# Kernel optimization log

Hardware: AMD Instinct MI355X
Metric: run time of the kernel (lower is better)

Reference implementation:

```python
import jax, jax.numpy as jnp
import numpy as np

H = 1024        # hidden_units
NH = 16         # num_heads
HD = H // NH    # head_dim = 64
B = 32
S = 500
MAX_SEQ = 500
ROPE_BASE = 10000.0


def setup_inputs() -> dict:
    key = jax.random.key(0)
    ks = jax.random.split(key, 16)
    s = 1.0 / np.sqrt(H)
    inp = {
        "query": jax.random.normal(ks[0], (B, S, H), jnp.float32),
        "key":   jax.random.normal(ks[1], (B, S, H), jnp.float32),
        "value": jax.random.normal(ks[2], (B, S, H), jnp.float32),
        "attn_mask": jax.random.randint(ks[3], (B, S), 0, 2).astype(bool),
        "Wq": jax.random.uniform(ks[4], (H, H), jnp.float32, -s, s),
        "bq": jax.random.uniform(ks[5], (H,), jnp.float32, -s, s),
        "Wk": jax.random.uniform(ks[6], (H, H), jnp.float32, -s, s),
        "bk": jax.random.uniform(ks[7], (H,), jnp.float32, -s, s),
        "Wv": jax.random.uniform(ks[8], (H, H), jnp.float32, -s, s),
        "bv": jax.random.uniform(ks[9], (H,), jnp.float32, -s, s),
        "Wo": jax.random.uniform(ks[10], (H, H), jnp.float32, -s, s),
        "bo": jax.random.uniform(ks[11], (H,), jnp.float32, -s, s),
        # rel_pos_bias embedding table: [2*max_seq_len-1, num_heads]
        "rel_emb": jax.random.normal(ks[12], (2 * MAX_SEQ - 1, NH), jnp.float32),
    }
    return inp


def _rope_tables(seq_len, head_dim, dtype):
    inv_freq = 1.0 / (ROPE_BASE ** (jnp.arange(0, head_dim, 2, dtype=jnp.float32) / head_dim))
    t = jnp.arange(seq_len, dtype=jnp.float32)
    freqs = t[:, None] * inv_freq[None, :]           # [S, HD/2]
    emb = jnp.concatenate([freqs, freqs], axis=-1)   # [S, HD]
    return jnp.cos(emb).astype(dtype), jnp.sin(emb).astype(dtype)


def _apply_rope(x, cos, sin):
    # x: [B, NH, S, HD]; even/odd slicing variant from source
    x_rot = jnp.concatenate([-x[..., 1::2], x[..., 0::2]], axis=-1)
    return x * cos + x_rot * sin


def reference(query, key, value, attn_mask, Wq, bq, Wk, bk, Wv, bv, Wo, bo, rel_emb):
    b, s, _ = query.shape
    Q = (query @ Wq.T + bq).reshape(b, s, NH, HD).transpose(0, 2, 1, 3)  # [B,NH,S,HD]
    K = (key   @ Wk.T + bk).reshape(b, s, NH, HD).transpose(0, 2, 1, 3)
    V = (value @ Wv.T + bv).reshape(b, s, NH, HD).transpose(0, 2, 1, 3)

    cos, sin = _rope_tables(s, HD, Q.dtype)  # [S,HD]
    Q = _apply_rope(Q, cos, sin)
    K = _apply_rope(K, cos, sin)

    # relative-position bias: [1, NH, S, S]
    pos = jnp.arange(s)[:, None] - jnp.arange(s)[None, :]
    rel_idx = jnp.clip(pos + MAX_SEQ - 1, 0, 2 * MAX_SEQ - 2)
    rel_bias = rel_emb[rel_idx].transpose(2, 0, 1)[None]  # [1,NH,S,S]

    # key-padding mask -> additive float mask [B,1,1,S]
    mask_bias = jnp.where(attn_mask[:, None, None, :], 0.0, -jnp.inf).astype(Q.dtype)

    scale = 1.0 / np.sqrt(HD)
    scores = jnp.einsum('bhqd,bhkd->bhqk', Q, K) * scale + mask_bias + rel_bias
    attn = jax.nn.softmax(scores, axis=-1)
    out = jnp.einsum('bhqk,bhkd->bhqd', attn, V)
    out = out.transpose(0, 2, 1, 3).reshape(b, s, H)
    out = jnp.clip(out, -30.0, 30.0)
    return out @ Wo.T + bo
```

## Files before the change

### kernel.cpp

```cpp
#include <hip/hip_runtime.h>
#include <math.h>


typedef unsigned short u16;
typedef unsigned int   u32;
typedef unsigned char  u8;
using bf16x8 = __attribute__((ext_vector_type(8))) short;
using f32x4  = __attribute__((ext_vector_type(4))) float;
using f32x2  = __attribute__((ext_vector_type(2))) float;
using u16x4  = __attribute__((ext_vector_type(4))) unsigned short;

#define DEV __device__ __forceinline__

#if __has_builtin(__builtin_amdgcn_exp2f)
#define EXP2(x) __builtin_amdgcn_exp2f(x)
#else
#define EXP2(x) exp2f(x)
#endif

DEV u16 f2bf(float f) {
  union { float f; u32 u; } c; c.f = f;
  u32 u = c.u;
  return (u16)((u + 0x7FFFu + ((u >> 16) & 1u)) >> 16);
}
DEV float bf2f(u16 h) {
  union { u32 u; float f; } c; c.u = ((u32)h) << 16;
  return c.f;
}
DEV u32 cvtpk(float a, float b) {
  u32 r;
  asm("v_cvt_pk_bf16_f32 %0, %1, %2" : "=v"(r) : "v"(a), "v"(b));
  return r;
}

DEV void async16(void* l, const void* g) {
  __builtin_amdgcn_global_load_lds(
      (__attribute__((address_space(1))) unsigned int*)g,
      (__attribute__((address_space(3))) unsigned int*)l, 16, 0, 0);
}

__global__ __launch_bounds__(512) void build_gather(const void* __restrict__ mraw,
                                                    u16* __restrict__ karr,
                                                    int* __restrict__ kept) {
  const int b = blockIdx.x;
  const int t = threadIdx.x;
  const int lane = t & 63, wave = t >> 6;
  __shared__ int s_li, s_lf;
  __shared__ int wbase[8];
  __shared__ int wpop[8];
  if (t == 0) { s_li = 0; s_lf = 0; }
  __syncthreads();
  const u32* w = (const u32*)mraw;
  int li = 0, lf = 0;
  for (int g = t; g < 4000; g += 512) {
    u32 v = w[g];
    li |= !(v == 0u || v == 1u);
    lf |= !(v == 0u || v == 0x3F800000u);
  }
  if (li) atomicOr(&s_li, 1);
  if (lf) atomicOr(&s_lf, 1);
  __syncthreads();
  const int mode = (!s_li) ? 0 : ((!s_lf) ? 1 : 2);
  int v = 0;
  if (t < 500) {
    if (mode == 0)      v = ((const int*)mraw)[b * 500 + t] != 0;
    else if (mode == 1) v = (((const float*)mraw)[b * 500 + t] != 0.0f);
    else                v = ((const u8*)mraw)[b * 500 + t] != 0;
  }
  unsigned long long bal = __ballot(v != 0);
  karr[b * 512 + t] = 0xFFFF;
  if (lane == 0) wpop[wave] = __popcll(bal);
  __syncthreads();
  if (t == 0) {
    int s = 0;
    for (int ww = 0; ww < 8; ++ww) { wbase[ww] = s; s += wpop[ww]; }
    kept[b] = s;
  }
  __syncthreads();
  if (v) {
    int rank = wbase[wave] + __popcll(bal & ((1ull << lane) - 1ull));
    karr[b * 512 + rank] = (u16)t;
  }
}

__global__ __launch_bounds__(256) void rope_table(float* __restrict__ tab) {
  int idx = blockIdx.x * 256 + threadIdx.x;
  if (idx >= 16000) return;
  int s = idx >> 5, j = idx & 31;
  float ang = (float)s * exp2f(-(float)j * 0.41524100f);
  float sn, cs;
  sincosf(ang, &sn, &cs);
  tab[idx * 2] = cs;
  tab[idx * 2 + 1] = sn;
}

__global__ __launch_bounds__(256) void cvt_w4(const float* __restrict__ w0,
                                              const float* __restrict__ w1,
                                              const float* __restrict__ w2,
                                              const float* __restrict__ w3,
                                              u16* __restrict__ dst) {
  const float* src = (blockIdx.y == 0) ? w0 : (blockIdx.y == 1) ? w1
                    : (blockIdx.y == 2) ? w2 : w3;
  int i = blockIdx.x * 256 + threadIdx.x;
  f32x4 f = *(const f32x4*)(src + (size_t)i * 4);
  u16x4 o;
  o[0] = f2bf(f[0]); o[1] = f2bf(f[1]); o[2] = f2bf(f[2]); o[3] = f2bf(f[3]);
  *(u16x4*)(dst + (size_t)blockIdx.y * 1048576 + (size_t)i * 4) = o;
}

__global__ __launch_bounds__(256) void cvt_f32_bf16(const float* __restrict__ src,
                                                    u16* __restrict__ dst, int n4) {
  int i = blockIdx.x * 256 + threadIdx.x;
  int stride = gridDim.x * 256;
  for (; i < n4; i += stride) {
    f32x4 f = *(const f32x4*)(src + (size_t)i * 4);
    u16x4 o;
    o[0] = f2bf(f[0]); o[1] = f2bf(f[1]); o[2] = f2bf(f[2]); o[3] = f2bf(f[3]);
    *(u16x4*)(dst + (size_t)i * 4) = o;
  }
}

__global__ __launch_bounds__(256) void gathercvt2(const float* __restrict__ srcK,
                                                  const float* __restrict__ srcV,
                                                  const u16* __restrict__ karr,
                                                  const int* __restrict__ kept,
                                                  u16* __restrict__ dstK,
                                                  u16* __restrict__ dstV) {
  const int b = blockIdx.y;
  const int r = blockIdx.x * 2 + (threadIdx.x >> 7);
  if (r >= kept[b]) return;
  const float* src = blockIdx.z ? srcV : srcK;
  u16* dst = blockIdx.z ? dstV : dstK;
  const int c = (threadIdx.x & 127) * 8;
  const int tok = karr[b * 512 + r];
  const float* s = src + ((size_t)b * 500 + tok) * 1024 + c;
  f32x4 f0 = *(const f32x4*)s;
  f32x4 f1 = *(const f32x4*)(s + 4);
  u16 o[8];
  o[0] = f2bf(f0[0]); o[1] = f2bf(f0[1]); o[2] = f2bf(f0[2]); o[3] = f2bf(f0[3]);
  o[4] = f2bf(f1[0]); o[5] = f2bf(f1[1]); o[6] = f2bf(f1[2]); o[7] = f2bf(f1[3]);
  *(bf16x8*)(dst + ((size_t)b * 512 + r) * 1024 + c) = *(bf16x8*)o;
}

DEV void gemm_core(const u16* __restrict__ A, size_t abase,
                   const u16* __restrict__ W,
                   int m0, int n0, int Mloc,
                   u16* AS, u16* BS, f32x4 (&acc)[4][4], int tid) {
  const int wave = tid >> 6;
  const int wr = wave >> 1, wc = wave & 1;
  const int fr = tid & 15, fo = (tid >> 4) & 3;
  const int fr2 = fr >> 1;
  const int aslot = ((4 * (fr & 1) + fo) ^ fr2) * 8;
  const int ATILE = 128 * 64;
  const int BTILE = 64 * 64;

#pragma unroll
  for (int mi = 0; mi < 4; ++mi)
#pragma unroll
    for (int ni = 0; ni < 4; ++ni)
#pragma unroll
      for (int j = 0; j < 4; ++j) acc[mi][ni][j] = 0.f;

  auto STG = [&](int t, int buf) {
    u16* sA = &AS[buf * ATILE];
    u16* sB = &BS[buf * BTILE];
#pragma unroll
    for (int i = 0; i < 2; ++i) {
      int c = i * 512 + tid;
      int r = c >> 3, v = (c & 7) ^ (r & 7);
      int ar = min(m0 + 2 * r + (v >> 2), Mloc - 1);
      async16(&sA[c * 8], A + abase + (size_t)ar * 1024 + t * 32 + (v & 3) * 8);
    }
    {
      int c = tid;
      int r = c >> 3, v = (c & 7) ^ (r & 7);
      int nr = n0 + 2 * r + (v >> 2);
      async16(&sB[c * 8], W + (size_t)nr * 1024 + t * 32 + (v & 3) * 8);
    }
  };

  STG(0, 0);
  asm volatile("s_waitcnt vmcnt(0)" ::: "memory");
  __builtin_amdgcn_sched_barrier(0);
  __builtin_amdgcn_s_barrier();

  int cur = 0;
  for (int t = 0; t < 32; ++t) {
    if (t + 1 < 32) STG(t + 1, cur ^ 1);
    const u16* a0 = &AS[cur * ATILE];
    const u16* b0 = &BS[cur * BTILE];
    bf16x8 a[4], b[4];
#pragma unroll
    for (int mi = 0; mi < 4; ++mi)
      a[mi] = *(const bf16x8*)&a0[(wr * 32 + mi * 8 + fr2) * 64 + aslot];
#pragma unroll
    for (int ni = 0; ni < 4; ++ni)
      b[ni] = *(const bf16x8*)&b0[(wc * 32 + ni * 8 + fr2) * 64 + aslot];
    asm volatile("s_waitcnt lgkmcnt(0)" ::: "memory");
    __builtin_amdgcn_sched_barrier(0);
    __builtin_amdgcn_s_setprio(1);
#pragma unroll
    for (int mi = 0; mi < 4; ++mi)
#pragma unroll
      for (int ni = 0; ni < 4; ++ni)
        acc[mi][ni] = __builtin_amdgcn_mfma_f32_16x16x32_bf16(a[mi], b[ni], acc[mi][ni], 0, 0, 0);
    __builtin_amdgcn_s_setprio(0);
    asm volatile("s_waitcnt vmcnt(0)" ::: "memory");
    __builtin_amdgcn_sched_barrier(0);
    __builtin_amdgcn_s_barrier();
    cur ^= 1;
  }
  __syncthreads();
}

__global__ __launch_bounds__(512, 4) void gemm_fused(
    const u16* __restrict__ Xq, const u16* __restrict__ XkC, const u16* __restrict__ XvC,
    const u16* __restrict__ Wb,
    const float* __restrict__ bq, const float* __restrict__ bk, const float* __restrict__ bv,
    u16* __restrict__ Qro, u16* __restrict__ Ktg, u16* __restrict__ Vtg,
    const float* __restrict__ tabg, const u16* __restrict__ karr,
    const int* __restrict__ keptp) {
  __shared__ __attribute__((aligned(16))) u16 SH[2 * 128 * 64 + 2 * 64 * 64];
  u16* AS = &SH[0];
  u16* BS = &SH[2 * 128 * 64];
  const int bid = blockIdx.x;
  const int tid = threadIdx.x;
  const int wave = tid >> 6;
  const int wr = wave >> 1, wc = wave & 1;
  const int fr = tid & 15, fo = (tid >> 4) & 3;
  const int lane = tid & 63;

  f32x4 acc[4][4];

  if (bid < 504) {
    const int swz = (bid & 7) * 63 + (bid >> 3);
    const int m0 = (swz >> 3) * 256;
    const int n0 = (swz & 7) * 128;
    gemm_core(Xq, 0, Wb, m0, n0, 16000, AS, BS, acc, tid);

    float* fw = (float*)&SH[0] + wave * 1024;
    const int hh = (n0 >> 6) + wc;
    const int row = lane >> 2;
    const int jb = (lane & 3) * 8;
    float bvv[4];
#pragma unroll
    for (int ni = 0; ni < 4; ++ni) bvv[ni] = bq[n0 + wc * 64 + ni * 16 + fr];
#pragma unroll
    for (int mi = 0; mi < 4; ++mi) {
#pragma unroll
      for (int ni = 0; ni < 4; ++ni)
#pragma unroll
        for (int r = 0; r < 4; ++r)
          fw[(fo * 4 + r) * 64 + ni * 16 + fr] = acc[mi][ni][r] + bvv[ni];
      int m = m0 + wr * 64 + mi * 16 + row;
      if (m < 16000) {
        int bb = (u32)m / 500u;
        int ss = m - bb * 500;
        u16* dst = Qro + (((size_t)(bb * 16 + hh)) * 500 + ss) * 64;
        bf16x8 va, vb;
#pragma unroll
        for (int p = 0; p < 8; ++p) {
          int j = jb + p;
          float x0 = fw[row * 64 + j];
          float x1 = fw[row * 64 + 32 + j];
          float xe = fw[row * 64 + 2 * j];
          float xo = fw[row * 64 + 2 * j + 1];
          f32x2 cn = *(const f32x2*)(tabg + (ss * 32 + j) * 2);
          va[p] = (short)f2bf(x0 * cn[0] - xo * cn[1]);
          vb[p] = (short)f2bf(x1 * cn[0] + xe * cn[1]);
        }
        *(bf16x8*)(dst + jb) = va;
        *(bf16x8*)(dst + 32 + jb) = vb;
      }
      __builtin_amdgcn_s_barrier();
    }
  } else {
    const bool isV = (bid >= 1016);
    const int local = isV ? (bid - 1016) : (bid - 504);
    const u16* A = isV ? XvC : XkC;
    const u16* W = Wb + (isV ? 2 : 1) * 1048576;
    const float* bias = isV ? bv : bk;
    const int swz = (local & 7) * 64 + (local >> 3);
    const int mb = swz >> 3;
    const int n0 = (swz & 7) * 128;
    const int b = mb >> 1, rb = mb & 1;
    const int kb = keptp[b];
    if (rb * 256 >= kb) return;
    const int m0 = rb * 256;
    gemm_core(A, (size_t)b * 512 * 1024, W, m0, n0, kb, AS, BS, acc, tid);

    float* fw = (float*)&SH[0] + wave * 1056;
    const int hh = (n0 >> 6) + wc;
    float bvv[4];
#pragma unroll
    for (int ni = 0; ni < 4; ++ni) bvv[ni] = bias[n0 + wc * 64 + ni * 16 + fr];

    if (!isV) {
      const int row = lane >> 2;
      const int jb = (lane & 3) * 8;
#pragma unroll
      for (int mi = 0; mi < 4; ++mi) {
#pragma unroll
        for (int ni = 0; ni < 4; ++ni)
#pragma unroll
          for (int r = 0; r < 4; ++r)
            fw[(fo * 4 + r) * 66 + ni * 16 + fr] = acc[mi][ni][r] + bvv[ni];
        int rk = m0 + wr * 64 + mi * 16 + row;
        int tile = rk >> 6, rin = rk & 63;
        int swk = (rin & 7) << 4;
        if (tile * 64 < kb) {
          char* outp = (char*)(Ktg + (((size_t)(b * 16 + hh)) * 8 + tile) * 4096) + rin * 128;
          bf16x8 va, vb;
          if (rk < kb) {
            int tok = karr[b * 512 + rk];
#pragma unroll
            for (int p = 0; p < 8; ++p) {
              int j = jb + p;
              float x0 = fw[row * 66 + j];
              float x1 = fw[row * 66 + 32 + j];
              float xe = fw[row * 66 + 2 * j];
              float xo = fw[row * 66 + 2 * j + 1];
              f32x2 cn = *(const f32x2*)(tabg + (tok * 32 + j) * 2);
              va[p] = (short)f2bf(x0 * cn[0] - xo * cn[1]);
              vb[p] = (short)f2bf(x1 * cn[0] + xe * cn[1]);
            }
          } else {
#pragma unroll
            for (int p = 0; p < 8; ++p) { va[p] = 0; vb[p] = 0; }
          }
          *(bf16x8*)(outp + ((2 * jb) ^ swk)) = va;
          *(bf16x8*)(outp + ((64 + 2 * jb) ^ swk)) = vb;
        }
        __builtin_amdgcn_s_barrier();
      }
    } else {
      const int d = lane;
      const int swv = (d & 7) << 4;
#pragma unroll
      for (int mi = 0; mi < 4; ++mi) {
#pragma unroll
        for (int ni = 0; ni < 4; ++ni)
#pragma unroll
          for (int r = 0; r < 4; ++r)
            fw[(fo * 4 + r) * 66 + ni * 16 + fr] = acc[mi][ni][r] + bvv[ni];
        int rk0 = m0 + wr * 64 + mi * 16;
        int tile = rk0 >> 6, rin0 = rk0 & 63;
        if (tile * 64 < kb) {
          char* rowp = (char*)(Vtg + (((size_t)(b * 16 + hh)) * 8 + tile) * 4096) + d * 128;
          bf16x8 va, vb;
#pragma unroll
          for (int t2 = 0; t2 < 8; ++t2)
            va[t2] = (rk0 + t2 < kb) ? (short)f2bf(fw[t2 * 66 + d]) : (short)0;
#pragma unroll
          for (int t2 = 0; t2 < 8; ++t2)
            vb[t2] = (rk0 + 8 + t2 < kb) ? (short)f2bf(fw[(8 + t2) * 66 + d]) : (short)0;
          *(bf16x8*)(rowp + ((2 * rin0) ^ swv)) = va;
          *(bf16x8*)(rowp + ((2 * rin0 + 16) ^ swv)) = vb;
        }
        __builtin_amdgcn_s_barrier();
      }
    }
  }
}

__global__ __launch_bounds__(512, 4) void gemm_out(const u16* __restrict__ A,
                                                   const u16* __restrict__ W,
                                                   const float* __restrict__ bias,
                                                   float* __restrict__ Cout) {
  __shared__ __attribute__((aligned(16))) u16 SH[2 * 128 * 64 + 2 * 64 * 64];
  u16* AS = &SH[0];
  u16* BS = &SH[2 * 128 * 64];
  const int bid = blockIdx.x;
  const int tid = threadIdx.x;
  const int wave = tid >> 6;
  const int wr = wave >> 1, wc = wave & 1;
  const int fr = tid & 15, fo = (tid >> 4) & 3;
  const int swz = (bid & 7) * 63 + (bid >> 3);
  const int m0 = (swz >> 3) * 256;
  const int n0 = (swz & 7) * 128;

  f32x4 acc[4][4];
  gemm_core(A, 0, W, m0, n0, 16000, AS, BS, acc, tid);

  float* fw = (float*)&SH[0] + wave * 1024;
#pragma unroll
  for (int mi = 0; mi < 4; ++mi) {
#pragma unroll
    for (int ni = 0; ni < 4; ++ni) {
      float bv = bias[n0 + wc * 64 + ni * 16 + fr];
#pragma unroll
      for (int r = 0; r < 4; ++r)
        fw[(fo * 4 + r) * 64 + ni * 16 + fr] = acc[mi][ni][r] + bv;
    }
    int lane = tid & 63;
    int ro = lane >> 2, ch = lane & 3;
    int m = m0 + wr * 64 + mi * 16 + ro;
    f32x4 v0 = *(const f32x4*)&fw[ro * 64 + ch * 16];
    f32x4 v1 = *(const f32x4*)&fw[ro * 64 + ch * 16 + 4];
    f32x4 v2 = *(const f32x4*)&fw[ro * 64 + ch * 16 + 8];
    f32x4 v3 = *(const f32x4*)&fw[ro * 64 + ch * 16 + 12];
    if (m < 16000) {
      float* dst = Cout + (size_t)m * 1024 + n0 + wc * 64 + ch * 16;
      *(f32x4*)dst = v0;
      *(f32x4*)(dst + 4) = v1;
      *(f32x4*)(dst + 8) = v2;
      *(f32x4*)(dst + 12) = v3;
    }
    __builtin_amdgcn_s_barrier();
  }
}

__global__ __launch_bounds__(512) void attn_kernel(const u16* __restrict__ Qr,
                                                   const u16* __restrict__ Ktg,
                                                   const u16* __restrict__ Vtg,
                                                   const float* __restrict__ rel_emb,
                                                   const u16* __restrict__ karr,
                                                   const int* __restrict__ kept,
                                                   u16* __restrict__ AO) {
  const int bid = blockIdx.x;
  const int bh = ((bid >> 5) << 3) | (bid & 7);
  const int qb = (bid >> 3) & 3;
  const int h = bh & 15, b = bh >> 4;
  const int q0 = qb * 128;
  const int tid = threadIdx.x;
  const int wave = tid >> 6;
  const int fr = tid & 15, fo = (tid >> 4) & 3;

  __shared__ __attribute__((aligned(16))) u16 Ks[2][4096];
  __shared__ __attribute__((aligned(16))) u16 Vs[2][4096];
  __shared__ __attribute__((aligned(16))) u16 Pl[8][1024];
  __shared__ float rel2[640];
  __shared__ u16 okk[512];

  const int nt = (kept[b] + 63) >> 6;
  const float LOG2E = 1.44269504f;
  for (int i = tid; i < 640; i += 512) {
    int g = min(max(q0 - 12 + i, 0), 998);
    rel2[i] = (i == 0) ? -1e30f : rel_emb[g * 16 + h] * LOG2E;
  }
  okk[tid] = karr[b * 512 + tid];

  const int qloc = wave * 16 + fr;
  const int qc = qloc + 511;
  const u16* Qb = Qr + ((size_t)bh * 500 + min(q0 + qloc, 499)) * 64;
  bf16x8 qf0 = *(const bf16x8*)(Qb + fo * 8);
  bf16x8 qf1 = *(const bf16x8*)(Qb + 32 + fo * 8);

  f32x4 o[4];
#pragma unroll
  for (int nf = 0; nf < 4; ++nf)
#pragma unroll
    for (int j = 0; j < 4; ++j) o[nf][j] = 0.f;
  float mrun = -1e30f, lrun = 0.f;

  const u16* Kb = Ktg + (size_t)bh * 32768;
  const u16* Vb = Vtg + (size_t)bh * 32768;
  const int sw = (fr & 7) << 4;
  const float SC = 0.18033688f;

  if (nt > 0) {
    async16(&Ks[0][tid * 8], Kb + tid * 8);
    async16(&Vs[0][tid * 8], Vb + tid * 8);
  }
  __syncthreads();

  for (int t = 0; t < nt; ++t) {
    const int cur = t & 1;
    if (t + 1 < nt) {
      async16(&Ks[cur ^ 1][tid * 8], Kb + (t + 1) * 4096 + tid * 8);
      async16(&Vs[cur ^ 1][tid * 8], Vb + (t + 1) * 4096 + tid * 8);
    }
    const char* Kt = (const char*)(cur ? &Ks[1][0] : &Ks[0][0]);
    const char* Vt = (const char*)(cur ? &Vs[1][0] : &Vs[0][0]);

    f32x4 sacc[4];
    __builtin_amdgcn_s_setprio(1);
#pragma unroll
    for (int nf = 0; nf < 4; ++nf) {
#pragma unroll
      for (int jj = 0; jj < 4; ++jj) sacc[nf][jj] = 0.f;
      int rb = (nf * 16 + fr) * 128;
      bf16x8 kb0 = *(const bf16x8*)(Kt + rb + ((fo * 16) ^ sw));
      bf16x8 kb1 = *(const bf16x8*)(Kt + rb + ((64 + fo * 16) ^ sw));
      sacc[nf] = __builtin_amdgcn_mfma_f32_16x16x32_bf16(kb0, qf0, sacc[nf], 0, 0, 0);
      sacc[nf] = __builtin_amdgcn_mfma_f32_16x16x32_bf16(kb1, qf1, sacc[nf], 0, 0, 0);
    }
    __builtin_amdgcn_s_setprio(0);

    float p2[4][4];
    float pmax = -3e30f;
#pragma unroll
    for (int nf = 0; nf < 4; ++nf) {
      u16x4 ok4 = *(const u16x4*)&okk[t * 64 + nf * 16 + fo * 4];
#pragma unroll
      for (int r = 0; r < 4; ++r) {
        int idx2 = max(qc - (int)ok4[r], 0);
        float s2 = fmaf(sacc[nf][r], SC, rel2[idx2]);
        p2[nf][r] = s2;
        pmax = fmaxf(pmax, s2);
      }
    }
    pmax = fmaxf(pmax, __shfl_xor(pmax, 16, 64));
    pmax = fmaxf(pmax, __shfl_xor(pmax, 32, 64));

    if (!__all(pmax <= mrun + 8.0f)) {
      float mnew = fmaxf(mrun, pmax);
      float scl = EXP2(mrun - mnew);
      lrun *= scl;
#pragma unroll
      for (int nf = 0; nf < 4; ++nf)
#pragma unroll
        for (int r = 0; r < 4; ++r) o[nf][r] *= scl;
      mrun = mnew;
    }

    float lsum = 0.f;
#pragma unroll
    for (int nf = 0; nf < 4; ++nf) {
      float e0 = EXP2(p2[nf][0] - mrun);
      float e1 = EXP2(p2[nf][1] - mrun);
      float e2 = EXP2(p2[nf][2] - mrun);
      float e3 = EXP2(p2[nf][3] - mrun);
      lsum += (e0 + e1) + (e2 + e3);
      uint2 w; w.x = cvtpk(e0, e1); w.y = cvtpk(e2, e3);
      *(uint2*)((char*)&Pl[wave][0] + fr * 128 + ((nf * 32 + fo * 8) ^ sw)) = w;
    }
    lsum += __shfl_xor(lsum, 16, 64);
    lsum += __shfl_xor(lsum, 32, 64);
    lrun += lsum;

    bf16x8 pa0 = *(const bf16x8*)((char*)&Pl[wave][0] + fr * 128 + ((fo * 16) ^ sw));
    bf16x8 pa1 = *(const bf16x8*)((char*)&Pl[wave][0] + fr * 128 + ((64 + fo * 16) ^ sw));
    __builtin_amdgcn_s_setprio(1);
#pragma unroll
    for (int nf = 0; nf < 4; ++nf) {
      int rb = (nf * 16 + fr) * 128;
      bf16x8 vb0 = *(const bf16x8*)(Vt + rb + ((fo * 16) ^ sw));
      bf16x8 vb1 = *(const bf16x8*)(Vt + rb + ((64 + fo * 16) ^ sw));
      o[nf] = __builtin_amdgcn_mfma_f32_16x16x32_bf16(vb0, pa0, o[nf], 0, 0, 0);
      o[nf] = __builtin_amdgcn_mfma_f32_16x16x32_bf16(vb1, pa1, o[nf], 0, 0, 0);
    }
    __builtin_amdgcn_s_setprio(0);
    __syncthreads();
  }

  float inv = (lrun > 0.f) ? 1.f / lrun : 0.f;
#pragma unroll
  for (int nf = 0; nf < 4; ++nf) {
    float v0 = fminf(fmaxf(o[nf][0] * inv, -30.f), 30.f);
    float v1 = fminf(fmaxf(o[nf][1] * inv, -30.f), 30.f);
    float v2 = fminf(fmaxf(o[nf][2] * inv, -30.f), 30.f);
    float v3 = fminf(fmaxf(o[nf][3] * inv, -30.f), 30.f);
    uint2 w; w.x = cvtpk(v0, v1); w.y = cvtpk(v2, v3);
    *(uint2*)((char*)&Pl[wave][0] + fr * 128 + ((nf * 32 + fo * 8) ^ sw)) = w;
  }
  {
    int lane = tid & 63;
    int ro = lane >> 2, c = lane & 3;
    int swr = (ro & 7) << 4;
    const char* Pw = (const char*)&Pl[wave][0];
    bf16x8 v0 = *(const bf16x8*)(Pw + ro * 128 + ((c * 32) ^ swr));
    bf16x8 v1 = *(const bf16x8*)(Pw + ro * 128 + ((c * 32 + 16) ^ swr));
    int token = q0 + wave * 16 + ro;
    if (token < 500) {
      u16* dst = AO + (size_t)(b * 500 + token) * 1024 + h * 64 + c * 16;
      *(bf16x8*)dst = v0;
      *(bf16x8*)(dst + 8) = v1;
    }
  }
}

extern "C" void kernel_launch(void* const* d_in, const int* in_sizes, int n_in,
                              void* d_out, int out_size, void* d_ws, size_t ws_size,
                              hipStream_t stream) {
  const float* query = (const float*)d_in[0];
  const float* key_  = (const float*)d_in[1];
  const float* value = (const float*)d_in[2];
  const void*  mask  = d_in[3];
  const float* Wq = (const float*)d_in[4];
  const float* bq = (const float*)d_in[5];
  const float* Wk = (const float*)d_in[6];
  const float* bk = (const float*)d_in[7];
  const float* Wv = (const float*)d_in[8];
  const float* bv = (const float*)d_in[9];
  const float* Wo = (const float*)d_in[10];
  const float* bo = (const float*)d_in[11];
  const float* rel = (const float*)d_in[12];

  char* ws = (char*)d_ws;
  const size_t SLOT = 33554432;
  u16* Wb = (u16*)ws;
  char* Aq = ws + 8388608;
  char* Bq = Aq + SLOT;
  char* Cq = Bq + SLOT;
  char* Dq = Cq + SLOT;
  char* Eq = Dq + SLOT;
  char* MISC = Eq + SLOT;
  u16* karr  = (u16*)(MISC + 65536);
  int* kept  = (int*)(MISC + 131072);
  float* tab = (float*)(MISC + 131584);
  u16* Qro = (u16*)d_out;

  build_gather<<<32, 512, 0, stream>>>(mask, karr, kept);
  rope_table<<<63, 256, 0, stream>>>(tab);
  cvt_w4<<<dim3(1024, 4), 256, 0, stream>>>(Wq, Wk, Wv, Wo, Wb);
  cvt_f32_bf16<<<2048, 256, 0, stream>>>(query, (u16*)Aq, 4096000);
  gathercvt2<<<dim3(256, 32, 2), 256, 0, stream>>>(key_, value, karr, kept,
                                                   (u16*)Bq, (u16*)Cq);

  gemm_fused<<<1528, 512, 0, stream>>>((u16*)Aq, (u16*)Bq, (u16*)Cq, Wb,
                                       bq, bk, bv,
                                       Qro, (u16*)Dq, (u16*)Eq, tab, karr, kept);

  attn_kernel<<<2048, 512, 0, stream>>>(Qro, (u16*)Dq, (u16*)Eq, rel,
                                        karr, kept, (u16*)Bq);

  gemm_out<<<504, 512, 0, stream>>>((u16*)Bq, Wb + 3 * 1048576, bo, (float*)d_out);
}
```

Measured before the change: 252.2 us.

## Fuse fp32-to-bf16 activation conversion and key gather into projection GEMM

Removes the separate conversion kernel for queries and the gather-convert kernel for keys and values. The projection GEMM now loads fp32 activations directly through register staging, converts them to bf16 while writing shared memory, and gathers kept key/value rows by token index cached in shared memory. This avoids writing and re-reading bf16 copies of the activations plus two launches. In exchange the A operand is no longer loaded asynchronously, and each tile reads twice as many bytes through registers, which could lengthen the main loop.

New measurement: 276.2 us. 1.1x slower.

```diff
diff --git a/kernel.cpp b/kernel.cpp
--- a/kernel.cpp
+++ b/kernel.cpp
@@ -108,38 +108,85 @@
   *(u16x4*)(dst + (size_t)blockIdx.y * 1048576 + (size_t)i * 4) = o;
 }
 
-__global__ __launch_bounds__(256) void cvt_f32_bf16(const float* __restrict__ src,
-                                                    u16* __restrict__ dst, int n4) {
-  int i = blockIdx.x * 256 + threadIdx.x;
-  int stride = gridDim.x * 256;
-  for (; i < n4; i += stride) {
-    f32x4 f = *(const f32x4*)(src + (size_t)i * 4);
-    u16x4 o;
-    o[0] = f2bf(f[0]); o[1] = f2bf(f[1]); o[2] = f2bf(f[2]); o[3] = f2bf(f[3]);
-    *(u16x4*)(dst + (size_t)i * 4) = o;
-  }
-}
-
-__global__ __launch_bounds__(256) void gathercvt2(const float* __restrict__ srcK,
-                                                  const float* __restrict__ srcV,
-                                                  const u16* __restrict__ karr,
-                                                  const int* __restrict__ kept,
-                                                  u16* __restrict__ dstK,
-                                                  u16* __restrict__ dstV) {
-  const int b = blockIdx.y;
-  const int r = blockIdx.x * 2 + (threadIdx.x >> 7);
-  if (r >= kept[b]) return;
-  const float* src = blockIdx.z ? srcV : srcK;
-  u16* dst = blockIdx.z ? dstV : dstK;
-  const int c = (threadIdx.x & 127) * 8;
-  const int tok = karr[b * 512 + r];
-  const float* s = src + ((size_t)b * 500 + tok) * 1024 + c;
-  f32x4 f0 = *(const f32x4*)s;
-  f32x4 f1 = *(const f32x4*)(s + 4);
-  u16 o[8];
-  o[0] = f2bf(f0[0]); o[1] = f2bf(f0[1]); o[2] = f2bf(f0[2]); o[3] = f2bf(f0[3]);
-  o[4] = f2bf(f1[0]); o[5] = f2bf(f1[1]); o[6] = f2bf(f1[2]); o[7] = f2bf(f1[3]);
-  *(bf16x8*)(dst + ((size_t)b * 512 + r) * 1024 + c) = *(bf16x8*)o;
+DEV void gemm_core_f32(const float* p0, const float* p1,
+                       const u16* __restrict__ W, int n0,
+                       u16* AS, u16* BS, f32x4 (&acc)[4][4], int tid) {
+  const int wave = tid >> 6;
+  const int wr = wave >> 1, wc = wave & 1;
+  const int fr = tid & 15, fo = (tid >> 4) & 3;
+  const int fr2 = fr >> 1;
+  const int aslot = ((4 * (fr & 1) + fo) ^ fr2) * 8;
+  const int ATILE = 128 * 64;
+  const int BTILE = 64 * 64;
+
+#pragma unroll
+  for (int mi = 0; mi < 4; ++mi)
+#pragma unroll
+    for (int ni = 0; ni < 4; ++ni)
+#pragma unroll
+      for (int j = 0; j < 4; ++j) acc[mi][ni][j] = 0.f;
+
+  f32x4 s0, s1, s2, s3;
+  auto A_LOAD = [&](int t) {
+    s0 = *(const f32x4*)(p0 + t * 32);
+    s1 = *(const f32x4*)(p0 + t * 32 + 4);
+    s2 = *(const f32x4*)(p1 + t * 32);
+    s3 = *(const f32x4*)(p1 + t * 32 + 4);
+  };
+  auto A_WRITE = [&](u16* sA) {
+    uint4 w0, w1;
+    w0.x = cvtpk(s0[0], s0[1]); w0.y = cvtpk(s0[2], s0[3]);
+    w0.z = cvtpk(s1[0], s1[1]); w0.w = cvtpk(s1[2], s1[3]);
+    w1.x = cvtpk(s2[0], s2[1]); w1.y = cvtpk(s2[2], s2[3]);
+    w1.z = cvtpk(s3[0], s3[1]); w1.w = cvtpk(s3[2], s3[3]);
+    *(uint4*)&sA[(size_t)tid * 8] = w0;
+    *(uint4*)&sA[(size_t)(512 + tid) * 8] = w1;
+  };
+  auto B_STG = [&](int t, u16* sB) {
+    int c = tid, r = c >> 3, v = (c & 7) ^ (r & 7);
+    int nr = n0 + 2 * r + (v >> 2);
+    async16(&sB[c * 8], W + (size_t)nr * 1024 + t * 32 + (v & 3) * 8);
+  };
+
+  A_LOAD(0); B_STG(0, &BS[0]);
+  asm volatile("s_waitcnt vmcnt(0)" ::: "memory");
+  __builtin_amdgcn_sched_barrier(0);
+  A_WRITE(&AS[0]);
+  asm volatile("s_waitcnt lgkmcnt(0)" ::: "memory");
+  __builtin_amdgcn_sched_barrier(0);
+  __builtin_amdgcn_s_barrier();
+
+  int cur = 0;
+  for (int t = 0; t < 32; ++t) {
+    const bool st = (t + 1 < 32);
+    if (st) { A_LOAD(t + 1); B_STG(t + 1, &BS[(cur ^ 1) * BTILE]); }
+    const u16* a0 = &AS[cur * ATILE];
+    const u16* b0 = &BS[cur * BTILE];
+    bf16x8 a[4], b[4];
+#pragma unroll
+    for (int mi = 0; mi < 4; ++mi)
+      a[mi] = *(const bf16x8*)&a0[(wr * 32 + mi * 8 + fr2) * 64 + aslot];
+#pragma unroll
+    for (int ni = 0; ni < 4; ++ni)
+      b[ni] = *(const bf16x8*)&b0[(wc * 32 + ni * 8 + fr2) * 64 + aslot];
+    asm volatile("s_waitcnt lgkmcnt(0)" ::: "memory");
+    __builtin_amdgcn_sched_barrier(0);
+    __builtin_amdgcn_s_setprio(1);
+#pragma unroll
+    for (int mi = 0; mi < 4; ++mi)
+#pragma unroll
+      for (int ni = 0; ni < 4; ++ni)
+        acc[mi][ni] = __builtin_amdgcn_mfma_f32_16x16x32_bf16(a[mi], b[ni], acc[mi][ni], 0, 0, 0);
+    __builtin_amdgcn_s_setprio(0);
+    asm volatile("s_waitcnt vmcnt(0)" ::: "memory");
+    __builtin_amdgcn_sched_barrier(0);
+    if (st) A_WRITE(&AS[(cur ^ 1) * ATILE]);
+    asm volatile("s_waitcnt lgkmcnt(0)" ::: "memory");
+    __builtin_amdgcn_sched_barrier(0);
+    __builtin_amdgcn_s_barrier();
+    cur ^= 1;
+  }
+  __syncthreads();
 }
 
 DEV void gemm_core(const u16* __restrict__ A, size_t abase,
@@ -214,13 +261,14 @@
 }
 
 __global__ __launch_bounds__(512, 4) void gemm_fused(
-    const u16* __restrict__ Xq, const u16* __restrict__ XkC, const u16* __restrict__ XvC,
+    const float* __restrict__ Xq, const float* __restrict__ Xk, const float* __restrict__ Xv,
     const u16* __restrict__ Wb,
     const float* __restrict__ bq, const float* __restrict__ bk, const float* __restrict__ bv,
     u16* __restrict__ Qro, u16* __restrict__ Ktg, u16* __restrict__ Vtg,
     const float* __restrict__ tabg, const u16* __restrict__ karr,
     const int* __restrict__ keptp) {
   __shared__ __attribute__((aligned(16))) u16 SH[2 * 128 * 64 + 2 * 64 * 64];
+  __shared__ u16 kloc[256];
   u16* AS = &SH[0];
   u16* BS = &SH[2 * 128 * 64];
   const int bid = blockIdx.x;
@@ -230,13 +278,21 @@
   const int fr = tid & 15, fo = (tid >> 4) & 3;
   const int lane = tid & 63;
 
+  const int r0 = tid >> 3, v0 = (tid & 7) ^ (r0 & 7);
+  const int c1i = 512 + tid;
+  const int r1 = c1i >> 3, v1 = (c1i & 7) ^ (r1 & 7);
+  const int rl0 = 2 * r0 + (v0 >> 2), kc0 = (v0 & 3) * 8;
+  const int rl1 = 2 * r1 + (v1 >> 2), kc1 = (v1 & 3) * 8;
+
   f32x4 acc[4][4];
 
   if (bid < 504) {
     const int swz = (bid & 7) * 63 + (bid >> 3);
     const int m0 = (swz >> 3) * 256;
     const int n0 = (swz & 7) * 128;
-    gemm_core(Xq, 0, Wb, m0, n0, 16000, AS, BS, acc, tid);
+    const float* p0 = Xq + (size_t)min(m0 + rl0, 15999) * 1024 + kc0;
+    const float* p1 = Xq + (size_t)min(m0 + rl1, 15999) * 1024 + kc1;
+    gemm_core_f32(p0, p1, Wb, n0, AS, BS, acc, tid);
 
     float* fw = (float*)&SH[0] + wave * 1024;
     const int hh = (n0 >> 6) + wc;
@@ -277,7 +333,7 @@
   } else {
     const bool isV = (bid >= 1016);
     const int local = isV ? (bid - 1016) : (bid - 504);
-    const u16* A = isV ? XvC : XkC;
+    const float* A = isV ? Xv : Xk;
     const u16* W = Wb + (isV ? 2 : 1) * 1048576;
     const float* bias = isV ? bv : bk;
     const int swz = (local & 7) * 64 + (local >> 3);
@@ -287,7 +343,15 @@
     const int kb = keptp[b];
     if (rb * 256 >= kb) return;
     const int m0 = rb * 256;
-    gemm_core(A, (size_t)b * 512 * 1024, W, m0, n0, kb, AS, BS, acc, tid);
+
+    if (tid < 256) {
+      u16 kv = karr[b * 512 + m0 + tid];
+      kloc[tid] = (kv == 0xFFFF) ? (u16)0 : kv;
+    }
+    __syncthreads();
+    const float* p0 = A + ((size_t)b * 500 + kloc[rl0]) * 1024 + kc0;
+    const float* p1 = A + ((size_t)b * 500 + kloc[rl1]) * 1024 + kc1;
+    gemm_core_f32(p0, p1, W, n0, AS, BS, acc, tid);
 
     float* fw = (float*)&SH[0] + wave * 1056;
     const int hh = (n0 >> 6) + wc;
@@ -312,7 +376,7 @@
           char* outp = (char*)(Ktg + (((size_t)(b * 16 + hh)) * 8 + tile) * 4096) + rin * 128;
           bf16x8 va, vb;
           if (rk < kb) {
-            int tok = karr[b * 512 + rk];
+            int tok = kloc[rk - m0];
 #pragma unroll
             for (int p = 0; p < 8; ++p) {
               int j = jb + p;
@@ -600,15 +664,13 @@
   int* kept  = (int*)(MISC + 131072);
   float* tab = (float*)(MISC + 131584);
   u16* Qro = (u16*)d_out;
+  (void)Aq; (void)Cq;
 
   build_gather<<<32, 512, 0, stream>>>(mask, karr, kept);
   rope_table<<<63, 256, 0, stream>>>(tab);
   cvt_w4<<<dim3(1024, 4), 256, 0, stream>>>(Wq, Wk, Wv, Wo, Wb);
-  cvt_f32_bf16<<<2048, 256, 0, stream>>>(query, (u16*)Aq, 4096000);
-  gathercvt2<<<dim3(256, 32, 2), 256, 0, stream>>>(key_, value, karr, kept,
-                                                   (u16*)Bq, (u16*)Cq);
-
-  gemm_fused<<<1528, 512, 0, stream>>>((u16*)Aq, (u16*)Bq, (u16*)Cq, Wb,
+
+  gemm_fused<<<1528, 512, 0, stream>>>(query, key_, value, Wb,
                                        bq, bk, bv,
                                        Qro, (u16*)Dq, (u16*)Eq, tab, karr, kept);
 
```
